# Performance work log

Measured on AMD Instinct MI355X. Metric: run time of the kernel, lower is better.

Reference implementation:

```python
import jax, jax.numpy as jnp
import numpy as np

D_MODEL = 1024
N_HEADS = 16
HEAD_DIM = D_MODEL // N_HEADS
NEG_INF = -1e30


def _rotary(v):
    # v: [B, H, T, hd]. Original module rotates each (even, odd) pair by 90 deg:
    # out[..., 2i] = -v[..., 2i+1]; out[..., 2i+1] = v[..., 2i]
    v2 = v.reshape(*v.shape[:-1], HEAD_DIM // 2, 2)
    return jnp.stack([-v2[..., 1], v2[..., 0]], axis=-1).reshape(v.shape)


def setup_inputs() -> dict:
    key = jax.random.key(0)
    ks = jax.random.split(key, 9)
    B, T, D = 2, 2048, D_MODEL
    s = 1.0 / np.sqrt(D)
    inp = {
        "x": jax.random.normal(ks[0], (B, T, D), dtype=jnp.float32),
        "Wq_w": jax.random.normal(ks[1], (D, D), dtype=jnp.float32) * s,
        "Wq_b": jnp.zeros((D,), dtype=jnp.float32),
        "Wk_w": jax.random.normal(ks[2], (D, D), dtype=jnp.float32) * s,
        "Wk_b": jnp.zeros((D,), dtype=jnp.float32),
        "Wv_w": jax.random.normal(ks[3], (D, D), dtype=jnp.float32) * s,
        "Wv_b": jnp.zeros((D,), dtype=jnp.float32),
        "Wo_w": jax.random.normal(ks[4], (D, D), dtype=jnp.float32) * s,
        "Wo_b": jnp.zeros((D,), dtype=jnp.float32),
    }
    # create_sparse_mask: block-diagonal True windows of size T//4
    window = T // 4
    blk = jnp.arange(T) // window
    inp["sparse_mask"] = blk[:, None] == blk[None, :]
    return inp


def reference(x, Wq_w, Wq_b, Wk_w, Wk_b, Wv_w, Wv_b, Wo_w, Wo_b, sparse_mask):
    B, T, D = x.shape
    H, hd = N_HEADS, HEAD_DIM

    def proj(w, b):  # [B,T,D] -> [B,H,T,hd]
        return (x @ w.T + b).reshape(B, T, H, hd).transpose(0, 2, 1, 3)

    q = _rotary(proj(Wq_w, Wq_b))
    k = _rotary(proj(Wk_w, Wk_b))
    v = proj(Wv_w, Wv_b)

    scores = jnp.einsum("bhqd,bhkd->bhqk", q, k) / jnp.sqrt(jnp.asarray(hd, x.dtype))
    causal = jnp.tril(jnp.ones((T, T), dtype=bool))
    allowed = sparse_mask & causal  # block-diagonal AND causal
    scores = jnp.where(allowed, scores, NEG_INF)
    attn = jax.nn.softmax(scores, axis=-1)  # dropout_p=0.1 omitted (eval mode)
    out = jnp.einsum("bhqk,bhkd->bhqd", attn, v)
    out = out.transpose(0, 2, 1, 3).reshape(B, T, D)
    return out @ Wo_w.T + Wo_b
```

## Files before the change

### kernel.cpp

```cpp
#include <hip/hip_runtime.h>
#include <hip/hip_bf16.h>
#include <stdint.h>

typedef __attribute__((ext_vector_type(4))) float f32x4;
typedef __attribute__((ext_vector_type(8))) __bf16 bf16x8;
typedef __attribute__((ext_vector_type(4))) unsigned short u16x4;
typedef __attribute__((ext_vector_type(8))) unsigned short u16x8;
typedef const __attribute__((address_space(1))) void* as1_cvp;
typedef __attribute__((address_space(3))) void* as3_vp;

#define LOG2E 1.44269504088896340736f

#define VMW0() asm volatile("s_waitcnt vmcnt(0)" ::: "memory")
#define VMW1() asm volatile("s_waitcnt vmcnt(1)" ::: "memory")
#define VMW2() asm volatile("s_waitcnt vmcnt(2)" ::: "memory")
#define VMW3() asm volatile("s_waitcnt vmcnt(3)" ::: "memory")
#define VMW4() asm volatile("s_waitcnt vmcnt(4)" ::: "memory")
#define VMW5() asm volatile("s_waitcnt vmcnt(5)" ::: "memory")
#define VMW6() asm volatile("s_waitcnt vmcnt(6)" ::: "memory")
#define BAR()  do { __builtin_amdgcn_sched_barrier(0); __builtin_amdgcn_s_barrier(); \
                    __builtin_amdgcn_sched_barrier(0); } while (0)

static __device__ __forceinline__ unsigned short f2bf(float f) {
  union { float f; unsigned int u; } c; c.f = f;
  unsigned int r = c.u + 0x7FFFu + ((c.u >> 16) & 1u);
  return (unsigned short)(r >> 16);
}

static __device__ __forceinline__ void gl_lds16(const void* g, void* l) {
  __builtin_amdgcn_global_load_lds((as1_cvp)(uintptr_t)g, (as3_vp)(uintptr_t)l, 16, 0, 0);
}

__global__ __launch_bounds__(256) void cvt_kernel(
    const float* __restrict__ x, const float* __restrict__ wq, const float* __restrict__ wk,
    const float* __restrict__ wv, const float* __restrict__ wo,
    unsigned short* __restrict__ xb, unsigned short* __restrict__ wqb,
    unsigned short* __restrict__ wkb, unsigned short* __restrict__ wvb,
    unsigned short* __restrict__ wob) {
  long e = ((long)blockIdx.x * 256 + threadIdx.x) * 8;
  const float* s; unsigned short* d; long o;
  if (e < 4194304)      { s = x;  d = xb;  o = e; }
  else if (e < 5242880) { s = wq; d = wqb; o = e - 4194304; }
  else if (e < 6291456) { s = wk; d = wkb; o = e - 5242880; }
  else if (e < 7340032) { s = wv; d = wvb; o = e - 6291456; }
  else                  { s = wo; d = wob; o = e - 7340032; }
  float4 a = *(const float4*)(s + o);
  float4 b = *(const float4*)(s + o + 4);
  u16x8 v;
  v[0] = f2bf(a.x); v[1] = f2bf(a.y); v[2] = f2bf(a.z); v[3] = f2bf(a.w);
  v[4] = f2bf(b.x); v[5] = f2bf(b.y); v[6] = f2bf(b.z); v[7] = f2bf(b.w);
  *(u16x8*)(d + o) = v;
}

__global__ __launch_bounds__(512, 2) void gemm_qkv8(
    const unsigned short* __restrict__ xb, const unsigned short* __restrict__ wcat,
    const float* __restrict__ bq, const float* __restrict__ bk, const float* __restrict__ bv,
    unsigned short* __restrict__ qo, unsigned short* __restrict__ ko,
    unsigned short* __restrict__ vto) {
  __shared__ __align__(16) char lds[114688];
  const int tid = threadIdx.x;
  const int lane = tid & 63, wid = tid >> 6;
  const int wm = wid >> 2, wn = wid & 3;
  const int c = lane & 15, g = lane >> 4;

  const int bid = blockIdx.x;
  const int swz = (bid & 7) * 32 + (bid >> 3);
  const int n0 = (swz & 15) * 192;
  const int m0 = (swz >> 4) << 8;

  const int srow = tid >> 3;
  const int coff = (((tid & 7) ^ (srow & 7)) << 4);
  const char* Ab = (const char*)xb;
  const char* Bb = (const char*)wcat;

  const int swzr0 = ((g ^ (c & 7)) << 4);
  const int swzr1 = (((4 | g) ^ (c & 7)) << 4);

  f32x4 acc[8][3] = {};
  bf16x8 afrA[2][2], afrB[2][2], bbf[3][2];

  auto STAGE = [&](int kt, int unit) {
    char* db = lds + (kt & 1) * 57344;
    const char* gp; char* dst;
    if (unit < 3) {
      gp = Bb + ((long)(n0 + unit * 64 + srow) << 11) + (kt << 7) + coff;
      dst = db + 32768 + unit * 8192 + tid * 16;
    } else {
      const int u = unit - 3;
      gp = Ab + ((long)(m0 + u * 64 + srow) << 11) + (kt << 7) + coff;
      dst = db + u * 8192 + tid * 16;
    }
    gl_lds16(gp, dst);
  };
  auto RDA = [&](bf16x8 (&dst)[2][2], int bufb, int u) {
    const char* p = lds + bufb + (u << 13) + (((wm << 5) + c) << 7);
#pragma unroll
    for (int f = 0; f < 2; ++f) {
      dst[f][0] = *(const bf16x8*)(p + (f << 11) + swzr0);
      dst[f][1] = *(const bf16x8*)(p + (f << 11) + swzr1);
    }
  };
  auto RDB = [&](int bufb) {
#pragma unroll
    for (int nf = 0; nf < 3; ++nf) {
      const int rB = wn * 48 + (nf << 4) + c;
      const char* p = lds + bufb + 32768 + ((rB >> 6) << 13) + ((rB & 63) << 7);
      bbf[nf][0] = *(const bf16x8*)(p + swzr0);
      bbf[nf][1] = *(const bf16x8*)(p + swzr1);
    }
  };
  auto MM = [&](int u, const bf16x8 (&af)[2][2]) {
    __builtin_amdgcn_s_setprio(1);
#pragma unroll
    for (int f = 0; f < 2; ++f)
#pragma unroll
      for (int nf = 0; nf < 3; ++nf)
#pragma unroll
        for (int kf = 0; kf < 2; ++kf)
          acc[u * 2 + f][nf] = __builtin_amdgcn_mfma_f32_16x16x32_bf16(
              af[f][kf], bbf[nf][kf], acc[u * 2 + f][nf], 0, 0, 0);
    __builtin_amdgcn_s_setprio(0);
  };

#pragma unroll
  for (int uu = 0; uu < 7; ++uu) STAGE(0, uu);

#pragma unroll 1
  for (int kt = 0; kt < 15; ++kt) {
    const int bufb = (kt & 1) * 57344;
    STAGE(kt + 1, 0); STAGE(kt + 1, 1);
    VMW4(); BAR();
    RDB(bufb); RDA(afrA, bufb, 0); RDA(afrB, bufb, 1);
    MM(0, afrA);
    STAGE(kt + 1, 2); STAGE(kt + 1, 3);
    VMW5(); BAR();
    RDA(afrA, bufb, 2);
    MM(1, afrB);
    STAGE(kt + 1, 4); STAGE(kt + 1, 5);
    VMW6(); BAR();
    RDA(afrB, bufb, 3);
    MM(2, afrA);
    STAGE(kt + 1, 6);
    VMW3(); BAR();
    MM(3, afrB);
  }
  {
    const int bufb = 57344;
    VMW2(); BAR();
    RDB(bufb); RDA(afrA, bufb, 0); RDA(afrB, bufb, 1);
    MM(0, afrA);
    VMW1(); BAR();
    RDA(afrA, bufb, 2);
    MM(1, afrB);
    VMW0(); BAR();
    RDA(afrB, bufb, 3);
    MM(2, afrA);
    MM(3, afrB);
  }

#pragma unroll
  for (int nf = 0; nf < 3; ++nf) {
    const int n = n0 + wn * 48 + (nf << 4) + c;
    const int z = n >> 10, nn = n & 1023;
    const float bb_ = (z == 0 ? bq : z == 1 ? bk : bv)[nn];
    const float sc = (z == 0) ? 0.125f : 1.0f;
    const int h = nn >> 6, dd = nn & 63;
#pragma unroll
    for (int a = 0; a < 8; ++a) {
      const int mb = m0 + ((a >> 1) << 6) + (wm << 5) + ((a & 1) << 4) + (g << 2);
      const int b = mb >> 11, tt = mb & 2047;
      if (z < 2) {
        unsigned short* dst = (z == 0 ? qo : ko) +
            ((((long)(b << 4) + h) << 11) + tt) * 64 + dd;
#pragma unroll
        for (int j = 0; j < 4; ++j) dst[(long)j * 64] = f2bf((acc[a][nf][j] + bb_) * sc);
      } else {
        u16x4 pk;
#pragma unroll
        for (int j = 0; j < 4; ++j) pk[j] = f2bf(acc[a][nf][j] + bb_);
        *(u16x4*)(vto + ((((long)((b << 4) + h) << 6) + dd) << 11) + tt) = pk;
      }
    }
  }
}

__global__ __launch_bounds__(512, 2) void gemm_oproj8(
    const unsigned short* __restrict__ ab, const unsigned short* __restrict__ wob,
    const float* __restrict__ bo, float* __restrict__ out) {
  __shared__ __align__(16) char lds[65536];
  const int tid = threadIdx.x;
  const int lane = tid & 63, wid = tid >> 6;
  const int wm = wid >> 2, wn = wid & 3;
  const int c = lane & 15, g = lane >> 4;

  const int bid = blockIdx.x;
  const int swz = (bid & 7) * 32 + (bid >> 3);
  const int n0 = (swz & 7) << 7;
  const int m0 = (swz >> 3) << 7;

  const int srow = tid >> 3;
  const int coff = (((tid & 7) ^ (srow & 7)) << 4);
  const char* Ab = (const char*)ab;
  const char* Bb = (const char*)wob;

  const int swzr0 = ((g ^ (c & 7)) << 4);
  const int swzr1 = (((4 | g) ^ (c & 7)) << 4);

  f32x4 acc[4][2] = {};
  bf16x8 afrA[2][2], afrB[2][2], bbf[2][2];

  auto STAGE = [&](int kt, int unit) {
    char* db = lds + (kt & 1) * 32768;
    const char* gp;
    if (unit < 2) gp = Ab + ((long)(m0 + unit * 64 + srow) << 11) + (kt << 7) + coff;
    else          gp = Bb + ((long)(n0 + (unit - 2) * 64 + srow) << 11) + (kt << 7) + coff;
    gl_lds16(gp, db + unit * 8192 + tid * 16);
  };
  auto RDA = [&](bf16x8 (&dst)[2][2], int bufb, int u) {
    const char* p = lds + bufb + (((u << 6) + (wm << 5) + c) << 7);
#pragma unroll
    for (int f = 0; f < 2; ++f) {
      dst[f][0] = *(const bf16x8*)(p + (f << 11) + swzr0);
      dst[f][1] = *(const bf16x8*)(p + (f << 11) + swzr1);
    }
  };
  auto RDB = [&](int bufb) {
#pragma unroll
    for (int nf = 0; nf < 2; ++nf) {
      const char* p = lds + bufb + 16384 + (((nf << 6) + (wn << 4) + c) << 7);
      bbf[nf][0] = *(const bf16x8*)(p + swzr0);
      bbf[nf][1] = *(const bf16x8*)(p + swzr1);
    }
  };
  auto MM = [&](int u, const bf16x8 (&af)[2][2]) {
    __builtin_amdgcn_s_setprio(1);
#pragma unroll
    for (int f = 0; f < 2; ++f)
#pragma unroll
      for (int nf = 0; nf < 2; ++nf)
#pragma unroll
        for (int kf = 0; kf < 2; ++kf)
          acc[u * 2 + f][nf] = __builtin_amdgcn_mfma_f32_16x16x32_bf16(
              af[f][kf], bbf[nf][kf], acc[u * 2 + f][nf], 0, 0, 0);
    __builtin_amdgcn_s_setprio(0);
  };

  STAGE(0, 0); STAGE(0, 2); STAGE(0, 3); STAGE(0, 1);

#pragma unroll 1
  for (int kt = 0; kt < 15; ++kt) {
    const int bufb = (kt & 1) * 32768;
    STAGE(kt + 1, 0); STAGE(kt + 1, 2);
    VMW2(); BAR();
    RDB(bufb); RDA(afrA, bufb, 0); RDA(afrB, bufb, 1);
    MM(0, afrA);
    STAGE(kt + 1, 3); STAGE(kt + 1, 1);
    BAR();
    MM(1, afrB);
  }
  {
    VMW0(); BAR();
    RDB(32768); RDA(afrA, 32768, 0); RDA(afrB, 32768, 1);
    MM(0, afrA);
    MM(1, afrB);
  }

#pragma unroll
  for (int nf = 0; nf < 2; ++nf) {
    const int n = n0 + (nf << 6) + (wn << 4) + c;
    const float bb = bo[n];
#pragma unroll
    for (int a = 0; a < 4; ++a) {
      const int mb = m0 + ((a >> 1) << 6) + (wm << 5) + ((a & 1) << 4) + (g << 2);
#pragma unroll
      for (int j = 0; j < 4; ++j)
        out[((long)(mb + j) << 10) + n] = acc[a][nf][j] + bb;
    }
  }
}

__global__ __launch_bounds__(512) void attn_kernel(
    const unsigned short* __restrict__ qg, const unsigned short* __restrict__ kg,
    const unsigned short* __restrict__ vtg, unsigned short* __restrict__ og) {
  __shared__ __align__(16) char kv_s[3][16384];
  __shared__ __align__(16) char p_s[8][2304];

  const int bx = blockIdx.x, bh = blockIdx.y;
  const int qt = ((bx & 3) << 2) + 3 - (bx >> 2);
  const int tid = threadIdx.x;
  const int lane = tid & 63, w = tid >> 6;
  const int c = lane & 15, g = lane >> 4;
  const int q0 = qt << 7;
  const int wstart = q0 & ~511;
  const int nt = ((q0 - wstart) >> 6) + 2;

  const unsigned short* qrow = qg + (((long)bh << 11) + q0 + (w << 4) + c) * 64;
  bf16x8 qa0 = *(const bf16x8*)(qrow + (g << 3));
  bf16x8 qa1 = *(const bf16x8*)(qrow + (g << 3) + 32);

  float m_run = -3.0e38f, l_run = 0.0f;
  f32x4 oacc[4] = {};

  const int sr = tid >> 3;
  const int jx16 = (((tid & 7) ^ (sr & 7)) << 4);
  const char* kbase = (const char*)kg + ((((long)bh << 11) + sr) << 7) + jx16;
  const char* vbase = (const char*)vtg + ((((long)bh << 6) + sr) << 12) + jx16;
  const int t16 = tid << 4;

  auto STAGEKV = [&](int kv0, int bsel) {
    char* dst = kv_s[bsel];
    gl_lds16(kbase + ((long)kv0 << 7), dst + t16);
    gl_lds16(vbase + ((long)kv0 << 1), dst + 8192 + t16);
  };

  STAGEKV(wstart, 0);
  STAGEKV(wstart + 64, 1);

  int rsel = 0, ssel = 2;
  for (int t = 0; t < nt; ++t) {
    if (t + 2 < nt) {
      STAGEKV(wstart + ((t + 2) << 6), ssel);
      VMW4();
    } else if (t + 1 < nt) {
      VMW2();
    } else {
      VMW0();
    }
    BAR();

    const char* kb_ = kv_s[rsel];
    const char* vb_ = kv_s[rsel] + 8192;
    const int kv0 = wstart + (t << 6);

    f32x4 sacc[4] = {};
    __builtin_amdgcn_s_setprio(1);
#pragma unroll
    for (int mf = 0; mf < 4; ++mf) {
      const int kr = (mf << 4) + c;
      const char* kp = kb_ + (kr << 7);
      bf16x8 k0 = *(const bf16x8*)(kp + ((g ^ (kr & 7)) << 4));
      bf16x8 k1 = *(const bf16x8*)(kp + (((4 | g) ^ (kr & 7)) << 4));
      sacc[mf] = __builtin_amdgcn_mfma_f32_16x16x32_bf16(k0, qa0, sacc[mf], 0, 0, 0);
      sacc[mf] = __builtin_amdgcn_mfma_f32_16x16x32_bf16(k1, qa1, sacc[mf], 0, 0, 0);
    }
    __builtin_amdgcn_s_setprio(0);

    const int dkv = kv0 - q0;
    if (dkv > (w << 4) - 64) {
      const int qrel = (w << 4) + c;
#pragma unroll
      for (int mf = 0; mf < 4; ++mf)
#pragma unroll
        for (int j = 0; j < 4; ++j)
          if (dkv + (mf << 4) + (g << 2) + j > qrel) sacc[mf][j] = -3.0e38f;
    }

    float pmax = -3.0e38f;
#pragma unroll
    for (int mf = 0; mf < 4; ++mf)
#pragma unroll
      for (int j = 0; j < 4; ++j) pmax = fmaxf(pmax, sacc[mf][j]);
    pmax = fmaxf(pmax, __shfl_xor(pmax, 16));
    pmax = fmaxf(pmax, __shfl_xor(pmax, 32));

    const float m_new = fmaxf(m_run, pmax);
    float lsum = 0.0f;
#pragma unroll
    for (int mf = 0; mf < 4; ++mf)
#pragma unroll
      for (int j = 0; j < 4; ++j) {
        const float p = __builtin_amdgcn_exp2f((sacc[mf][j] - m_new) * LOG2E);
        sacc[mf][j] = p;
        lsum += p;
      }
    lsum += __shfl_xor(lsum, 16);
    lsum += __shfl_xor(lsum, 32);
    const float alpha = __builtin_amdgcn_exp2f((m_run - m_new) * LOG2E);
    l_run = l_run * alpha + lsum;
    m_run = m_new;

    {
      char* pw = p_s[w] + c * 144;
#pragma unroll
      for (int mf = 0; mf < 4; ++mf) {
        u16x4 pk;
#pragma unroll
        for (int j = 0; j < 4; ++j) pk[j] = f2bf(sacc[mf][j]);
        *(u16x4*)(pw + (mf << 5) + (g << 3)) = pk;
      }
    }

#pragma unroll
    for (int j = 0; j < 4; ++j) {
      const float aj = __shfl(alpha, (g << 2) + j);
#pragma unroll
      for (int nf = 0; nf < 4; ++nf) oacc[nf][j] *= aj;
    }

    const char* pr = p_s[w] + c * 144;
    __builtin_amdgcn_s_setprio(1);
#pragma unroll
    for (int kk = 0; kk < 2; ++kk) {
      bf16x8 pa = *(const bf16x8*)(pr + (kk << 6) + (g << 4));
#pragma unroll
      for (int nf = 0; nf < 4; ++nf) {
        const int vr = (nf << 4) + c;
        bf16x8 vb = *(const bf16x8*)(vb_ + (vr << 7) +
                                     ((((kk << 2) | g) ^ (vr & 7)) << 4));
        oacc[nf] = __builtin_amdgcn_mfma_f32_16x16x32_bf16(pa, vb, oacc[nf], 0, 0, 0);
      }
    }
    __builtin_amdgcn_s_setprio(0);
    BAR();

    rsel = (rsel == 2) ? 0 : rsel + 1;
    ssel = (ssel == 2) ? 0 : ssel + 1;
  }

  const int b = bh >> 4, h = bh & 15;
#pragma unroll
  for (int j = 0; j < 4; ++j) {
    const float linv = 1.0f / __shfl(l_run, (g << 2) + j);
    const int trow = q0 + (w << 4) + (g << 2) + j;
    unsigned short* dst = og + ((((long)(b << 11)) + trow) << 10) + (h << 6);
#pragma unroll
    for (int nf = 0; nf < 4; ++nf)
      dst[(nf << 4) + c] = f2bf(oacc[nf][j] * linv);
  }
}

extern "C" void kernel_launch(void* const* d_in, const int* in_sizes, int n_in,
                              void* d_out, int out_size, void* d_ws, size_t ws_size,
                              hipStream_t stream) {
  const float* x  = (const float*)d_in[0];
  const float* wq = (const float*)d_in[1];
  const float* bq = (const float*)d_in[2];
  const float* wk = (const float*)d_in[3];
  const float* bk = (const float*)d_in[4];
  const float* wv = (const float*)d_in[5];
  const float* bv = (const float*)d_in[6];
  const float* wo = (const float*)d_in[7];
  const float* bo = (const float*)d_in[8];

  char* ws = (char*)d_ws;
  unsigned short* xb    = (unsigned short*)(ws);
  unsigned short* wqb   = (unsigned short*)(ws + 8388608);
  unsigned short* wkb   = (unsigned short*)(ws + 10485760);
  unsigned short* wvb   = (unsigned short*)(ws + 12582912);
  unsigned short* wob   = (unsigned short*)(ws + 14680064);
  unsigned short* qb    = (unsigned short*)(ws + 16777216);
  unsigned short* kb    = (unsigned short*)(ws + 25165824);
  unsigned short* vtb   = (unsigned short*)(ws + 33554432);
  unsigned short* attnb = xb;

  cvt_kernel<<<4096, 256, 0, stream>>>(x, wq, wk, wv, wo, xb, wqb, wkb, wvb, wob);
  gemm_qkv8<<<256, 512, 0, stream>>>(xb, wqb, bq, bk, bv, qb, kb, vtb);
  attn_kernel<<<dim3(16, 32), 512, 0, stream>>>(qb, kb, vtb, attnb);
  gemm_oproj8<<<256, 512, 0, stream>>>(attnb, wob, bo, (float*)d_out);
}
```

Before: 79.46 us.

## Coarsen QKV GEMM pipeline phases and remap blocks for XCD-local tiles

The QKV projection GEMM's main loop goes from four barrier-separated phases per k-step to two. Loads for the next tile are issued in larger batches and two MFMA groups run between barriers, with vmcnt waits adjusted to match. The block-to-tile mapping also changes so each XCD covers a contiguous 4x8 region of M and N tiles, which should improve L2 reuse. Fewer barriers mean less sync overhead, but larger issue batches could expose more load latency before the first compute group.

After: 79.54 us. About the same (+0.1%).

```diff
diff --git a/kernel.cpp b/kernel.cpp
--- a/kernel.cpp
+++ b/kernel.cpp
@@ -14,10 +14,9 @@
 #define VMW0() asm volatile("s_waitcnt vmcnt(0)" ::: "memory")
 #define VMW1() asm volatile("s_waitcnt vmcnt(1)" ::: "memory")
 #define VMW2() asm volatile("s_waitcnt vmcnt(2)" ::: "memory")
-#define VMW3() asm volatile("s_waitcnt vmcnt(3)" ::: "memory")
 #define VMW4() asm volatile("s_waitcnt vmcnt(4)" ::: "memory")
 #define VMW5() asm volatile("s_waitcnt vmcnt(5)" ::: "memory")
-#define VMW6() asm volatile("s_waitcnt vmcnt(6)" ::: "memory")
+#define VMW7() asm volatile("s_waitcnt vmcnt(7)" ::: "memory")
 #define BAR()  do { __builtin_amdgcn_sched_barrier(0); __builtin_amdgcn_s_barrier(); \
                     __builtin_amdgcn_sched_barrier(0); } while (0)
 
@@ -64,9 +63,9 @@
   const int c = lane & 15, g = lane >> 4;
 
   const int bid = blockIdx.x;
-  const int swz = (bid & 7) * 32 + (bid >> 3);
-  const int n0 = (swz & 15) * 192;
-  const int m0 = (swz >> 4) << 8;
+  const int xcd = bid & 7, idx = bid >> 3;
+  const int m0 = (((xcd >> 1) << 2) + (idx >> 3)) << 8;
+  const int n0 = (((xcd & 1) << 3) + (idx & 7)) * 192;
 
   const int srow = tid >> 3;
   const int coff = (((tid & 7) ^ (srow & 7)) << 4);
@@ -128,34 +127,23 @@
 #pragma unroll 1
   for (int kt = 0; kt < 15; ++kt) {
     const int bufb = (kt & 1) * 57344;
-    STAGE(kt + 1, 0); STAGE(kt + 1, 1);
-    VMW4(); BAR();
+    STAGE(kt + 1, 0); STAGE(kt + 1, 1); STAGE(kt + 1, 2);
+    VMW5(); BAR();
     RDB(bufb); RDA(afrA, bufb, 0); RDA(afrB, bufb, 1);
-    MM(0, afrA);
-    STAGE(kt + 1, 2); STAGE(kt + 1, 3);
-    VMW5(); BAR();
-    RDA(afrA, bufb, 2);
-    MM(1, afrB);
-    STAGE(kt + 1, 4); STAGE(kt + 1, 5);
-    VMW6(); BAR();
-    RDA(afrB, bufb, 3);
-    MM(2, afrA);
-    STAGE(kt + 1, 6);
-    VMW3(); BAR();
-    MM(3, afrB);
+    MM(0, afrA); MM(1, afrB);
+    STAGE(kt + 1, 3); STAGE(kt + 1, 4); STAGE(kt + 1, 5); STAGE(kt + 1, 6);
+    VMW7(); BAR();
+    RDA(afrA, bufb, 2); RDA(afrB, bufb, 3);
+    MM(2, afrA); MM(3, afrB);
   }
   {
     const int bufb = 57344;
     VMW2(); BAR();
     RDB(bufb); RDA(afrA, bufb, 0); RDA(afrB, bufb, 1);
-    MM(0, afrA);
-    VMW1(); BAR();
-    RDA(afrA, bufb, 2);
-    MM(1, afrB);
+    MM(0, afrA); MM(1, afrB);
     VMW0(); BAR();
-    RDA(afrB, bufb, 3);
-    MM(2, afrA);
-    MM(3, afrB);
+    RDA(afrA, bufb, 2); RDA(afrB, bufb, 3);
+    MM(2, afrA); MM(3, afrB);
   }
 
 #pragma unroll
```
